# Kernel optimization log

Measured on AMD Instinct MI355X. Metric: run time of the kernel, lower is better.

The kernel has to match this reference:

```python
import jax, jax.numpy as jnp
import numpy as np

IN_FEATURES = 128
OUT_FEATURES = 128


def setup_inputs() -> dict:
    key = jax.random.key(0)
    k1, k2, k3 = jax.random.split(key, 3)
    h_i = jax.random.normal(k1, (IN_FEATURES,), dtype=jnp.float32)
    h_j = jax.random.normal(k2, (200000, OUT_FEATURES), dtype=jnp.float32)
    a = jax.random.normal(k3, (IN_FEATURES + OUT_FEATURES, 1), dtype=jnp.float32)
    return {"h_i": h_i, "h_j": h_j, "a": a}


def reference(h_i, h_j, a):
    # e_n = dot(concat(h_i, h_j[n]), a) = h_i . a[:in] + h_j[n] . a[in:]
    a_i = a[:IN_FEATURES, 0]   # [in]
    a_j = a[IN_FEATURES:, 0]   # [out]
    logits = jnp.dot(h_i, a_i) + h_j @ a_j        # [N]
    attention = jax.nn.softmax(logits, axis=0)    # [N]
    # dropout is identity in eval mode (training=False)
    h_prime = attention @ h_j                     # [out]
    return jax.nn.elu(h_prime)                    # concat=True -> ELU
```

## Files before the change

### kernel.cpp

```cpp
#include <hip/hip_runtime.h>
#include <math.h>

#define COLS 128

__global__ __launch_bounds__(256) void gat_pass1(
    const float* __restrict__ hj, const float* __restrict__ a,
    float* __restrict__ pacc, float* __restrict__ pm, float* __restrict__ pl,
    int nrows, int nunits) {
  const int t    = threadIdx.x;
  const int wave = t >> 6;
  const int lane = t & 63;
  const int half = lane >> 5;
  const int sub  = lane & 31;
  const int uib  = wave * 2 + half;
  const int unit = blockIdx.x * 8 + uib;

  const float4 aj = ((const float4*)(a + COLS))[sub];

  float m = -INFINITY, l = 0.f;
  float ax = 0.f, ay = 0.f, az = 0.f, aw = 0.f;

  const int stride = nunits;
  int r = unit;

  for (; r + stride < nrows; r += 2 * stride) {
    const float4 v0 = ((const float4*)(hj + (size_t)r * COLS))[sub];
    const float4 v1 = ((const float4*)(hj + (size_t)(r + stride) * COLS))[sub];

    float p0 = v0.x * aj.x + v0.y * aj.y + v0.z * aj.z + v0.w * aj.w;
    #pragma unroll
    for (int off = 1; off <= 16; off <<= 1) p0 += __shfl_xor(p0, off, 64);
    if (p0 <= m) {
      const float w = __expf(p0 - m);
      l += w; ax += w * v0.x; ay += w * v0.y; az += w * v0.z; aw += w * v0.w;
    } else {
      const float alpha = __expf(m - p0);
      l = l * alpha + 1.f;
      ax = ax * alpha + v0.x; ay = ay * alpha + v0.y;
      az = az * alpha + v0.z; aw = aw * alpha + v0.w;
      m = p0;
    }

    float p1 = v1.x * aj.x + v1.y * aj.y + v1.z * aj.z + v1.w * aj.w;
    #pragma unroll
    for (int off = 1; off <= 16; off <<= 1) p1 += __shfl_xor(p1, off, 64);
    if (p1 <= m) {
      const float w = __expf(p1 - m);
      l += w; ax += w * v1.x; ay += w * v1.y; az += w * v1.z; aw += w * v1.w;
    } else {
      const float alpha = __expf(m - p1);
      l = l * alpha + 1.f;
      ax = ax * alpha + v1.x; ay = ay * alpha + v1.y;
      az = az * alpha + v1.z; aw = aw * alpha + v1.w;
      m = p1;
    }
  }
  for (; r < nrows; r += stride) {
    const float4 v0 = ((const float4*)(hj + (size_t)r * COLS))[sub];
    float p0 = v0.x * aj.x + v0.y * aj.y + v0.z * aj.z + v0.w * aj.w;
    #pragma unroll
    for (int off = 1; off <= 16; off <<= 1) p0 += __shfl_xor(p0, off, 64);
    if (p0 <= m) {
      const float w = __expf(p0 - m);
      l += w; ax += w * v0.x; ay += w * v0.y; az += w * v0.z; aw += w * v0.w;
    } else {
      const float alpha = __expf(m - p0);
      l = l * alpha + 1.f;
      ax = ax * alpha + v0.x; ay = ay * alpha + v0.y;
      az = az * alpha + v0.z; aw = aw * alpha + v0.w;
      m = p0;
    }
  }

  __shared__ float sm[8], sl[8], se[8], sMb;
  __shared__ float sacc[8][COLS];
  ((float4*)sacc[uib])[sub] = make_float4(ax, ay, az, aw);
  if (sub == 0) { sm[uib] = m; sl[uib] = l; }
  __syncthreads();

  if (t < 8) {
    float Mb = sm[0];
    #pragma unroll
    for (int u = 1; u < 8; u++) Mb = fmaxf(Mb, sm[u]);
    se[t] = __expf(sm[t] - Mb);
    if (t == 0) sMb = Mb;
  }
  __syncthreads();

  if (t < COLS) {
    float s = 0.f;
    #pragma unroll
    for (int u = 0; u < 8; u++) s += se[u] * sacc[u][t];
    pacc[(size_t)blockIdx.x * COLS + t] = s;
  }
  if (t == 0) {
    float lb = 0.f;
    #pragma unroll
    for (int u = 0; u < 8; u++) lb += se[u] * sl[u];
    pm[blockIdx.x] = sMb;
    pl[blockIdx.x] = lb;
  }
}

__global__ __launch_bounds__(256) void gat_pass2(
    const float* __restrict__ pacc, const float* __restrict__ pm,
    const float* __restrict__ pl, float* __restrict__ out, int nblocks) {
  const int col = blockIdx.x;
  const int t   = threadIdx.x;
  __shared__ float sM[4], sz[4], sc[4];

  float local = -INFINITY;
  for (int b = t; b < nblocks; b += 256) local = fmaxf(local, pm[b]);
  #pragma unroll
  for (int off = 1; off < 64; off <<= 1) local = fmaxf(local, __shfl_xor(local, off, 64));
  if ((t & 63) == 0) sM[t >> 6] = local;
  __syncthreads();
  const float M = fmaxf(fmaxf(sM[0], sM[1]), fmaxf(sM[2], sM[3]));

  float zs = 0.f, cs = 0.f;
  for (int b = t; b < nblocks; b += 256) {
    const float e = __expf(pm[b] - M);
    zs += e * pl[b];
    cs += e * pacc[(size_t)b * COLS + col];
  }
  #pragma unroll
  for (int off = 1; off < 64; off <<= 1) {
    zs += __shfl_xor(zs, off, 64);
    cs += __shfl_xor(cs, off, 64);
  }
  if ((t & 63) == 0) { sz[t >> 6] = zs; sc[t >> 6] = cs; }
  __syncthreads();

  if (t == 0) {
    const float Z = sz[0] + sz[1] + sz[2] + sz[3];
    const float C = sc[0] + sc[1] + sc[2] + sc[3];
    const float h = C / Z;
    out[col] = h > 0.f ? h : expm1f(h);
  }
}

extern "C" void kernel_launch(void* const* d_in, const int* in_sizes, int n_in,
                              void* d_out, int out_size, void* d_ws, size_t ws_size,
                              hipStream_t stream) {
  const float* hj = (const float*)d_in[1];
  const float* a  = (const float*)d_in[2];
  float* out = (float*)d_out;

  const int nrows = in_sizes[1] / COLS;

  int nblocks = 2048;
  const size_t per_block = (COLS + 2) * sizeof(float);
  if (ws_size < (size_t)nblocks * per_block) {
    nblocks = (int)(ws_size / per_block);
    if (nblocks > 64) nblocks &= ~63;
    if (nblocks < 1) nblocks = 1;
  }
  const int nunits = nblocks * 8;

  float* pacc = (float*)d_ws;
  float* pm   = pacc + (size_t)nblocks * COLS;
  float* pl   = pm + nblocks;

  gat_pass1<<<nblocks, 256, 0, stream>>>(hj, a, pacc, pm, pl, nrows, nunits);
  gat_pass2<<<COLS, 256, 0, stream>>>(pacc, pm, pl, out, nblocks);
}
```

Baseline: 155.9 us.

## Fuse two passes via last-block atomic reduction and batch four rows per step

```diff
diff --git a/kernel.cpp b/kernel.cpp
--- a/kernel.cpp
+++ b/kernel.cpp
@@ -2,11 +2,13 @@
 #include <math.h>
 
 #define COLS 128
+#define NB   1024
 
-__global__ __launch_bounds__(256) void gat_pass1(
+__global__ __launch_bounds__(256) void gat_fused(
     const float* __restrict__ hj, const float* __restrict__ a,
     float* __restrict__ pacc, float* __restrict__ pm, float* __restrict__ pl,
-    int nrows, int nunits) {
+    unsigned int* __restrict__ cnt, float* __restrict__ out,
+    int nrows, int nblocks) {
   const int t    = threadIdx.x;
   const int wave = t >> 6;
   const int lane = t & 63;
@@ -14,65 +16,57 @@
   const int sub  = lane & 31;
   const int uib  = wave * 2 + half;
   const int unit = blockIdx.x * 8 + uib;
+  const int stride = nblocks * 8;
 
   const float4 aj = ((const float4*)(a + COLS))[sub];
 
   float m = -INFINITY, l = 0.f;
   float ax = 0.f, ay = 0.f, az = 0.f, aw = 0.f;
 
-  const int stride = nunits;
   int r = unit;
-
-  for (; r + stride < nrows; r += 2 * stride) {
+  for (; r + 3 * stride < nrows; r += 4 * stride) {
     const float4 v0 = ((const float4*)(hj + (size_t)r * COLS))[sub];
     const float4 v1 = ((const float4*)(hj + (size_t)(r + stride) * COLS))[sub];
+    const float4 v2 = ((const float4*)(hj + (size_t)(r + 2 * stride) * COLS))[sub];
+    const float4 v3 = ((const float4*)(hj + (size_t)(r + 3 * stride) * COLS))[sub];
 
     float p0 = v0.x * aj.x + v0.y * aj.y + v0.z * aj.z + v0.w * aj.w;
+    float p1 = v1.x * aj.x + v1.y * aj.y + v1.z * aj.z + v1.w * aj.w;
+    float p2 = v2.x * aj.x + v2.y * aj.y + v2.z * aj.z + v2.w * aj.w;
+    float p3 = v3.x * aj.x + v3.y * aj.y + v3.z * aj.z + v3.w * aj.w;
     #pragma unroll
-    for (int off = 1; off <= 16; off <<= 1) p0 += __shfl_xor(p0, off, 64);
-    if (p0 <= m) {
-      const float w = __expf(p0 - m);
-      l += w; ax += w * v0.x; ay += w * v0.y; az += w * v0.z; aw += w * v0.w;
-    } else {
-      const float alpha = __expf(m - p0);
-      l = l * alpha + 1.f;
-      ax = ax * alpha + v0.x; ay = ay * alpha + v0.y;
-      az = az * alpha + v0.z; aw = aw * alpha + v0.w;
-      m = p0;
+    for (int off = 1; off <= 16; off <<= 1) {
+      p0 += __shfl_xor(p0, off, 64);
+      p1 += __shfl_xor(p1, off, 64);
+      p2 += __shfl_xor(p2, off, 64);
+      p3 += __shfl_xor(p3, off, 64);
     }
-
-    float p1 = v1.x * aj.x + v1.y * aj.y + v1.z * aj.z + v1.w * aj.w;
-    #pragma unroll
-    for (int off = 1; off <= 16; off <<= 1) p1 += __shfl_xor(p1, off, 64);
-    if (p1 <= m) {
-      const float w = __expf(p1 - m);
-      l += w; ax += w * v1.x; ay += w * v1.y; az += w * v1.z; aw += w * v1.w;
-    } else {
-      const float alpha = __expf(m - p1);
-      l = l * alpha + 1.f;
-      ax = ax * alpha + v1.x; ay = ay * alpha + v1.y;
-      az = az * alpha + v1.z; aw = aw * alpha + v1.w;
-      m = p1;
-    }
+    const float mm = fmaxf(fmaxf(fmaxf(p0, p1), fmaxf(p2, p3)), m);
+    const float alpha = __expf(m - mm);
+    const float w0 = __expf(p0 - mm), w1 = __expf(p1 - mm);
+    const float w2 = __expf(p2 - mm), w3 = __expf(p3 - mm);
+    l  = l * alpha + ((w0 + w1) + (w2 + w3));
+    ax = ax * alpha + w0 * v0.x + w1 * v1.x + w2 * v2.x + w3 * v3.x;
+    ay = ay * alpha + w0 * v0.y + w1 * v1.y + w2 * v2.y + w3 * v3.y;
+    az = az * alpha + w0 * v0.z + w1 * v1.z + w2 * v2.z + w3 * v3.z;
+    aw = aw * alpha + w0 * v0.w + w1 * v1.w + w2 * v2.w + w3 * v3.w;
+    m = mm;
   }
   for (; r < nrows; r += stride) {
     const float4 v0 = ((const float4*)(hj + (size_t)r * COLS))[sub];
     float p0 = v0.x * aj.x + v0.y * aj.y + v0.z * aj.z + v0.w * aj.w;
     #pragma unroll
     for (int off = 1; off <= 16; off <<= 1) p0 += __shfl_xor(p0, off, 64);
-    if (p0 <= m) {
-      const float w = __expf(p0 - m);
-      l += w; ax += w * v0.x; ay += w * v0.y; az += w * v0.z; aw += w * v0.w;
-    } else {
-      const float alpha = __expf(m - p0);
-      l = l * alpha + 1.f;
-      ax = ax * alpha + v0.x; ay = ay * alpha + v0.y;
-      az = az * alpha + v0.z; aw = aw * alpha + v0.w;
-      m = p0;
-    }
+    const float mm = fmaxf(p0, m);
+    const float alpha = __expf(m - mm);
+    const float w0 = __expf(p0 - mm);
+    l  = l * alpha + w0;
+    ax = ax * alpha + w0 * v0.x; ay = ay * alpha + w0 * v0.y;
+    az = az * alpha + w0 * v0.z; aw = aw * alpha + w0 * v0.w;
+    m = mm;
   }
 
-  __shared__ float sm[8], sl[8], se[8], sMb;
+  __shared__ float sm[8], sl[8], seu[8], sMb;
   __shared__ float sacc[8][COLS];
   ((float4*)sacc[uib])[sub] = make_float4(ax, ay, az, aw);
   if (sub == 0) { sm[uib] = m; sl[uib] = l; }
@@ -82,7 +76,7 @@
     float Mb = sm[0];
     #pragma unroll
     for (int u = 1; u < 8; u++) Mb = fmaxf(Mb, sm[u]);
-    se[t] = __expf(sm[t] - Mb);
+    seu[t] = __expf(sm[t] - Mb);
     if (t == 0) sMb = Mb;
   }
   __syncthreads();
@@ -90,52 +84,62 @@
   if (t < COLS) {
     float s = 0.f;
     #pragma unroll
-    for (int u = 0; u < 8; u++) s += se[u] * sacc[u][t];
+    for (int u = 0; u < 8; u++) s += seu[u] * sacc[u][t];
     pacc[(size_t)blockIdx.x * COLS + t] = s;
   }
+  if (t == 0) { pm[blockIdx.x] = sMb; pl[blockIdx.x] = sl[0] * seu[0] + sl[1] * seu[1] + sl[2] * seu[2] + sl[3] * seu[3] + sl[4] * seu[4] + sl[5] * seu[5] + sl[6] * seu[6] + sl[7] * seu[7]; }
+
+  __threadfence();
+  __syncthreads();
+  __shared__ int sLast;
   if (t == 0) {
-    float lb = 0.f;
-    #pragma unroll
-    for (int u = 0; u < 8; u++) lb += se[u] * sl[u];
-    pm[blockIdx.x] = sMb;
-    pl[blockIdx.x] = lb;
+    const unsigned int old = atomicAdd(cnt, 1u);
+    sLast = (old == (unsigned int)nblocks - 1u);
   }
-}
+  __syncthreads();
+  if (!sLast) return;
+  __threadfence();
 
-__global__ __launch_bounds__(256) void gat_pass2(
-    const float* __restrict__ pacc, const float* __restrict__ pm,
-    const float* __restrict__ pl, float* __restrict__ out, int nblocks) {
-  const int col = blockIdx.x;
-  const int t   = threadIdx.x;
-  __shared__ float sM[4], sz[4], sc[4];
+  __shared__ float se[NB];
+  __shared__ float red[4];
+  __shared__ float sMZ[2];
+  __shared__ float chalf[2][COLS];
 
-  float local = -INFINITY;
-  for (int b = t; b < nblocks; b += 256) local = fmaxf(local, pm[b]);
+  float mx = -INFINITY;
+  for (int b = t; b < nblocks; b += 256) mx = fmaxf(mx, pm[b]);
   #pragma unroll
-  for (int off = 1; off < 64; off <<= 1) local = fmaxf(local, __shfl_xor(local, off, 64));
-  if ((t & 63) == 0) sM[t >> 6] = local;
+  for (int off = 1; off < 64; off <<= 1) mx = fmaxf(mx, __shfl_xor(mx, off, 64));
+  if (lane == 0) red[wave] = mx;
   __syncthreads();
-  const float M = fmaxf(fmaxf(sM[0], sM[1]), fmaxf(sM[2], sM[3]));
+  if (t == 0) sMZ[0] = fmaxf(fmaxf(red[0], red[1]), fmaxf(red[2], red[3]));
+  __syncthreads();
+  const float M = sMZ[0];
 
-  float zs = 0.f, cs = 0.f;
+  float zz = 0.f;
   for (int b = t; b < nblocks; b += 256) {
     const float e = __expf(pm[b] - M);
-    zs += e * pl[b];
-    cs += e * pacc[(size_t)b * COLS + col];
+    se[b] = e;
+    zz += e * pl[b];
   }
   #pragma unroll
-  for (int off = 1; off < 64; off <<= 1) {
-    zs += __shfl_xor(zs, off, 64);
-    cs += __shfl_xor(cs, off, 64);
-  }
-  if ((t & 63) == 0) { sz[t >> 6] = zs; sc[t >> 6] = cs; }
+  for (int off = 1; off < 64; off <<= 1) zz += __shfl_xor(zz, off, 64);
+  if (lane == 0) red[wave] = zz;
   __syncthreads();
+  if (t == 0) sMZ[1] = red[0] + red[1] + red[2] + red[3];
+  __syncthreads();
+  const float Z = sMZ[1];
 
-  if (t == 0) {
-    const float Z = sz[0] + sz[1] + sz[2] + sz[3];
-    const float C = sc[0] + sc[1] + sc[2] + sc[3];
-    const float h = C / Z;
-    out[col] = h > 0.f ? h : expm1f(h);
+  const int col = t & 127;
+  const int hh  = t >> 7;
+  float cs = 0.f;
+  #pragma unroll 4
+  for (int b = hh; b < nblocks; b += 2)
+    cs += se[b] * pacc[(size_t)b * COLS + col];
+  chalf[hh][col] = cs;
+  __syncthreads();
+  if (t < COLS) {
+    const float h = (chalf[0][t] + chalf[1][t]) / Z;
+    out[t] = h > 0.f ? h : expm1f(h);
   }
 }
 
@@ -148,19 +152,20 @@
 
   const int nrows = in_sizes[1] / COLS;
 
-  int nblocks = 2048;
+  int nblocks = NB;
   const size_t per_block = (COLS + 2) * sizeof(float);
-  if (ws_size < (size_t)nblocks * per_block) {
-    nblocks = (int)(ws_size / per_block);
+  if (ws_size < (size_t)nblocks * per_block + 256) {
+    nblocks = (int)((ws_size - 256) / per_block);
     if (nblocks > 64) nblocks &= ~63;
     if (nblocks < 1) nblocks = 1;
   }
-  const int nunits = nblocks * 8;
 
   float* pacc = (float*)d_ws;
   float* pm   = pacc + (size_t)nblocks * COLS;
   float* pl   = pm + nblocks;
+  size_t off = ((size_t)nblocks * (COLS + 2) * sizeof(float) + 255) & ~(size_t)255;
+  unsigned int* cnt = (unsigned int*)((char*)d_ws + off);
 
-  gat_pass1<<<nblocks, 256, 0, stream>>>(hj, a, pacc, pm, pl, nrows, nunits);
-  gat_pass2<<<COLS, 256, 0, stream>>>(pacc, pm, pl, out, nblocks);
+  hipMemsetAsync(cnt, 0, sizeof(unsigned int), stream);
+  gat_fused<<<nblocks, 256, 0, stream>>>(hj, a, pacc, pm, pl, cnt, out, nrows, nblocks);
 }
```

Result: slower. 278.7 us (+78.8%).
